# Kernel tuning notes

Measured on AMD Instinct MI355X. Metric: run time of the kernel, lower is better.

## Reference

```python
import jax, jax.numpy as jnp
import numpy as np

EPS = 1e-5  # torch BatchNorm default eps


def _bn(x, gamma, beta, axes):
    # training-mode batch norm over `axes`, channel dim is axis 1
    mean = jnp.mean(x, axis=axes, keepdims=True)
    var = jnp.var(x, axis=axes, keepdims=True)
    shape = [1] * x.ndim
    shape[1] = -1
    return (x - mean) * jax.lax.rsqrt(var + EPS) * gamma.reshape(shape) + beta.reshape(shape)


def setup_inputs() -> dict:
    B, C, N = 16, 512, 192
    S_RATIO, R_RATIO = 4, 8
    Cs, Cr = C // S_RATIO, C // R_RATIO  # 128, 64
    inter = N * Cr + C  # 12800
    key = jax.random.key(0)
    ks = jax.random.split(key, 6)

    def w(k, shp, fan):
        return jax.random.normal(k, shp, jnp.float32) * np.float32(np.sqrt(2.0 / fan))

    return {
        "inputs": jax.random.normal(ks[0], (B, C, N), jnp.float32),
        "retain": 0,
        "theta_w": w(ks[1], (Cs, C), Cs), "theta_b": jnp.zeros((Cs,), jnp.float32),
        "theta_g": jnp.ones((Cs,), jnp.float32), "theta_be": jnp.zeros((Cs,), jnp.float32),
        "phi_w": w(ks[2], (Cs, C), Cs), "phi_b": jnp.zeros((Cs,), jnp.float32),
        "phi_g": jnp.ones((Cs,), jnp.float32), "phi_be": jnp.zeros((Cs,), jnp.float32),
        "re_w": w(ks[3], (Cr, Cs), Cr), "re_b": jnp.zeros((Cr,), jnp.float32),
        "re_g": jnp.ones((Cr,), jnp.float32), "re_be": jnp.zeros((Cr,), jnp.float32),
        "att_w": w(ks[4], (C, inter), C), "att_b": jnp.zeros((C,), jnp.float32),
        "att_g": jnp.ones((C,), jnp.float32), "att_be": jnp.zeros((C,), jnp.float32),
    }


def reference(inputs, retain, theta_w, theta_b, theta_g, theta_be,
              phi_w, phi_b, phi_g, phi_be, re_w, re_b, re_g, re_be,
              att_w, att_b, att_g, att_be):
    B, C, N = inputs.shape
    xt = inputs.transpose(0, 2, 1)  # [B, N, C]

    # theta / phi pro_blocks: Linear -> BN1d (over B,N) -> ReLU, output [B, Cs, N]
    th = jax.nn.relu(_bn(jnp.einsum('bnc,oc->bon', xt, theta_w) + theta_b[None, :, None], theta_g, theta_be, (0, 2)))
    ph = jax.nn.relu(_bn(jnp.einsum('bnc,oc->bon', xt, phi_w) + phi_b[None, :, None], phi_g, phi_be, (0, 2)))
    th = th.transpose(0, 2, 1)  # [B, N, Cs]
    ph = ph.transpose(0, 2, 1)  # [B, N, Cs]

    # pairwise broadcast-diff: [B, N, N, Cs]
    diff = th[:, :, None, :] - ph[:, None, :, :]

    # pro_block1: Linear -> BN2d -> ReLU, then flatten to [B, N, N*Cr]
    rel = jnp.einsum('bijc,oc->boij', diff, re_w) + re_b[None, :, None, None]  # [B, Cr, N, N]
    rel = jax.nn.relu(_bn(rel, re_g, re_be, (0, 2, 3)))
    rel = rel.transpose(0, 2, 3, 1).reshape(B, N, -1)  # [B, N, N*Cr]

    # attention_generator: Linear -> BN1d -> sigmoid, output [B, C, N]
    cat = jnp.concatenate([xt, rel], axis=2)  # [B, N, C + N*Cr]
    att = jnp.einsum('bni,oi->bon', cat, att_w) + att_b[None, :, None]  # [B, C, N]
    att = jax.nn.sigmoid(_bn(att, att_g, att_be, (0, 2)))

    features = att * inputs  # [B, C, N]
    if retain:
        return features
    return jnp.sum(features, axis=2) / jnp.sum(att, axis=2)  # [B, C]
```

## Files before the change

kernel.cpp:

```cpp
#include <hip/hip_runtime.h>

#define BB 16
#define CC 512
#define NN 192
#define CS 128
#define CR 64
#define EPSF 1e-5f
#define PART (BB*CC*NN)

typedef __attribute__((ext_vector_type(8))) short short8;
typedef __attribute__((ext_vector_type(4))) float f32x4;
typedef __attribute__((ext_vector_type(4))) unsigned int uint4v;

#define OFF_LIN2  0
#define OFF_P2    786432
#define OFF_QT    983040
#define OFF_ATTP4 1179648
#define OFF_WBF   7471104
#define OFF_XT    10747904
#define OFF_ROWS  11534336
#define OFF_SPART 11567104

__device__ __forceinline__ unsigned pkbf(float a, float b){
  unsigned r; asm("v_cvt_pk_bf16_f32 %0, %1, %2" : "=v"(r) : "v"(a), "v"(b)); return r;
}

__device__ __forceinline__ void gload_lds16(const void* g, void* l){
  __builtin_amdgcn_global_load_lds(
      (const __attribute__((address_space(1))) unsigned int*)g,
      (__attribute__((address_space(3))) unsigned int*)l, 16, 0, 0);
}

__global__ __launch_bounds__(256) void kconvxt(
    const float* __restrict__ aw, const float* __restrict__ x,
    short* __restrict__ wbf, short* __restrict__ xT)
{
  __shared__ float Ts[64][65];
  if (blockIdx.x < 3200) {
    int t = blockIdx.x*256 + threadIdx.x;
    int o2 = t / 1600;
    int kk = (t - o2*1600) * 8;
    const float* src = &aw[o2*12800 + kk];
    float4 v0 = *reinterpret_cast<const float4*>(src);
    float4 v1 = *reinterpret_cast<const float4*>(src+4);
    uint4v w;
    w.x = pkbf(v0.x, v0.y); w.y = pkbf(v0.z, v0.w);
    w.z = pkbf(v1.x, v1.y); w.w = pkbf(v1.z, v1.w);
    *reinterpret_cast<uint4v*>(&wbf[o2*12800 + kk]) = w;
  } else {
    int bid = blockIdx.x - 3200;
    int nt = bid % 3; int ct = (bid/3) & 7; int b = bid / 24;
    int c0 = ct*64, n0 = nt*64;
    int tid = threadIdx.x;
    int col = tid & 63, r0 = tid >> 6;
    #pragma unroll
    for (int it = 0; it < 16; ++it){
      int r = r0 + it*4;
      Ts[r][col] = x[(b*CC + c0 + r)*NN + n0 + col];
    }
    __syncthreads();
    #pragma unroll
    for (int it = 0; it < 2; ++it){
      int cp = it*256 + tid;
      int nr = cp >> 3, cc8 = (cp & 7)*8;
      uint4v wv;
      wv.x = pkbf(Ts[cc8+0][nr], Ts[cc8+1][nr]);
      wv.y = pkbf(Ts[cc8+2][nr], Ts[cc8+3][nr]);
      wv.z = pkbf(Ts[cc8+4][nr], Ts[cc8+5][nr]);
      wv.w = pkbf(Ts[cc8+6][nr], Ts[cc8+7][nr]);
      *reinterpret_cast<uint4v*>(&xT[((b*NN) + n0 + nr)*CC + c0 + cc8]) = wv;
    }
  }
}

__global__ __launch_bounds__(256) void k1_lin(
    const float* __restrict__ x, const float* __restrict__ wth,
    const float* __restrict__ wph, float* __restrict__ lin2,
    float* __restrict__ spart)
{
  int bid = blockIdx.x;
  int nt = bid % 3; int ch = (bid/3) & 3; int b = (bid/12) & 15; int path = bid/192;
  int cs0 = ch*32, n0 = nt*64;
  const float* w = path ? wph : wth;
  int tid = threadIdx.x;
  int ty = tid >> 4, tx = tid & 15;
  __shared__ float Xs[32][64];
  __shared__ float Ws[32][36];
  float acc[2][4];
  #pragma unroll
  for (int i=0;i<2;++i)
    #pragma unroll
    for (int j=0;j<4;++j) acc[i][j]=0.f;
  for (int c0 = 0; c0 < CC; c0 += 32){
    __syncthreads();
    {
      int nn = tid & 63, cb = tid >> 6;
      #pragma unroll
      for (int it = 0; it < 8; ++it)
        Xs[cb + it*4][nn] = x[(b*CC + c0 + cb + it*4)*NN + n0 + nn];
    }
    {
      int cc = tid & 31, sb = tid >> 5;
      #pragma unroll
      for (int it = 0; it < 4; ++it)
        Ws[cc][sb + it*8] = w[(cs0 + sb + it*8)*CC + c0 + cc];
    }
    __syncthreads();
    #pragma unroll 8
    for (int cc = 0; cc < 32; ++cc){
      float w2[2], x4[4];
      w2[0] = Ws[cc][ty*2]; w2[1] = Ws[cc][ty*2+1];
      *reinterpret_cast<float4*>(x4) = *reinterpret_cast<const float4*>(&Xs[cc][tx*4]);
      #pragma unroll
      for (int i=0;i<2;++i)
        #pragma unroll
        for (int j=0;j<4;++j) acc[i][j] += w2[i]*x4[j];
    }
  }
  #pragma unroll
  for (int r = 0; r < 2; ++r){
    int cs = cs0 + ty*2 + r;
    float4 v = make_float4(acc[r][0],acc[r][1],acc[r][2],acc[r][3]);
    *reinterpret_cast<float4*>(&lin2[(b*256 + path*128 + cs)*NN + n0 + tx*4]) = v;
  }
  #pragma unroll
  for (int r = 0; r < 2; ++r){
    float s = acc[r][0]+acc[r][1]+acc[r][2]+acc[r][3];
    float q = acc[r][0]*acc[r][0]+acc[r][1]*acc[r][1]
            + acc[r][2]*acc[r][2]+acc[r][3]*acc[r][3];
    #pragma unroll
    for (int off=8; off; off>>=1){ s += __shfl_down(s,off,16); q += __shfl_down(q,off,16); }
    if (tx==0){
      int cs2 = path*128 + cs0 + ty*2 + r;
      spart[cs2*48 + b*3 + nt] = s;
      spart[12288 + cs2*48 + b*3 + nt] = q;
    }
  }
}

__global__ __launch_bounds__(256) void k3_gemm(
    const float* __restrict__ lin2, const float* __restrict__ spart,
    const float* __restrict__ tg, const float* __restrict__ tbe,
    const float* __restrict__ pg, const float* __restrict__ pbe,
    const float* __restrict__ rw,
    float* __restrict__ p2raw, float* __restrict__ qTraw,
    float* __restrict__ rows8)
{
  int bid = blockIdx.x;
  int ih = bid & 7; int b = (bid>>3) & 15; int path = bid >> 7;
  int i0 = ih*24;
  __shared__ float Ls[128][24];
  __shared__ float Ws[64][132];
  __shared__ float sscl[512];
  int tid = threadIdx.x;
  {
    int c2 = tid;
    float s=0.f, q=0.f;
    #pragma unroll 8
    for (int i=0;i<48;++i){ s += spart[c2*48+i]; q += spart[12288+c2*48+i]; }
    float mean = s * (1.f/3072.f);
    float var = q * (1.f/3072.f) - mean*mean;
    int pth = c2 >> 7, c = c2 & 127;
    float g  = pth ? pg[c]  : tg[c];
    float be = pth ? pbe[c] : tbe[c];
    float a = g * rsqrtf(var + EPSF);
    sscl[c2] = a; sscl[256+c2] = be - mean*a;
  }
  __syncthreads();
  #pragma unroll
  for (int it = 0; it < 3; ++it){
    int cp = it*256 + tid;
    int row = cp / 6, c4 = cp - row*6;
    float a = sscl[path*128 + row], d = sscl[256 + path*128 + row];
    float4 v = *reinterpret_cast<const float4*>(&lin2[(b*256 + path*128 + row)*NN + i0 + c4*4]);
    float4 r;
    r.x = fmaxf(a*v.x + d, 0.f); r.y = fmaxf(a*v.y + d, 0.f);
    r.z = fmaxf(a*v.z + d, 0.f); r.w = fmaxf(a*v.w + d, 0.f);
    *reinterpret_cast<float4*>(&Ls[row][c4*4]) = r;
  }
  #pragma unroll
  for (int it = 0; it < 8; ++it){
    int cp = it*256 + tid;
    int o = cp >> 5, c4 = cp & 31;
    *reinterpret_cast<float4*>(&Ws[o][c4*4]) =
      *reinterpret_cast<const float4*>(&rw[o*CS + c4*4]);
  }
  __syncthreads();
  int oy = tid >> 3, ix = tid & 7;
  float acc[2][3];
  #pragma unroll
  for (int r=0;r<2;++r)
    #pragma unroll
    for (int e=0;e<3;++e) acc[r][e]=0.f;
  #pragma unroll 4
  for (int c = 0; c < 128; ++c){
    float w2[2], l3[3];
    #pragma unroll
    for (int r=0;r<2;++r) w2[r] = Ws[oy*2+r][c];
    #pragma unroll
    for (int e=0;e<3;++e) l3[e] = Ls[c][ix*3+e];
    #pragma unroll
    for (int r=0;r<2;++r)
      #pragma unroll
      for (int e=0;e<3;++e) acc[r][e] += w2[r]*l3[e];
  }
  float* dst = path ? qTraw : p2raw;
  #pragma unroll
  for (int r=0;r<2;++r)
    #pragma unroll
    for (int e=0;e<3;++e)
      dst[(b*NN + i0 + ix*3 + e)*64 + oy*2 + r] = acc[r][e];
  #pragma unroll
  for (int r=0;r<2;++r){
    float s = acc[r][0]+acc[r][1]+acc[r][2];
    float q = acc[r][0]*acc[r][0]+acc[r][1]*acc[r][1]+acc[r][2]*acc[r][2];
    #pragma unroll
    for (int off=4; off; off>>=1){ s += __shfl_down(s,off,8); q += __shfl_down(q,off,8); }
    if (ix==0){
      int o = oy*2+r;
      int ri = (path*1024 + b*64 + o)*8 + ih;
      rows8[ri] = s; rows8[16384 + ri] = q;
    }
  }
}

__global__ __launch_bounds__(256) void k5_mfma(
    const short* __restrict__ wbf, const short* __restrict__ xT,
    const float* __restrict__ p2raw, const float* __restrict__ qTraw,
    const float* __restrict__ rows8,
    const float* __restrict__ rg, const float* __restrict__ rbe,
    float* __restrict__ attp4)
{
  int bid = blockIdx.x;
  int nt = bid & 1, mt = (bid >> 1) & 3, b = (bid >> 3) & 15, ks = bid >> 7;
  int o20 = mt*128, n0 = nt*96;
  int j0 = ks*48;

  int tid = threadIdx.x;
  int w = tid >> 6, lane = tid & 63;
  int wr = w >> 1, wc = w & 1;
  int l15 = lane & 15, l4 = lane >> 4;
  int cq = tid & 7;

  __shared__ __align__(16) short As[2][128*64];
  __shared__ __align__(16) short Bs[96*64];
  __shared__ __align__(16) float qall[48*64];
  __shared__ float srel[128];
  __shared__ float sred[4][5][64];

  {
    int o = tid & 63, g = tid >> 6;
    float sa=0,sb=0,saq=0,sbq=0,cross=0;
    #pragma unroll
    for (int bb=g*4; bb<g*4+4; ++bb){
      float ra=0, rb=0;
      #pragma unroll
      for (int ih=0; ih<8; ++ih){
        int ia = (bb*64+o)*8 + ih, ib = (1024 + bb*64+o)*8 + ih;
        ra += rows8[ia]; rb += rows8[ib];
        saq += rows8[16384 + ia]; sbq += rows8[16384 + ib];
      }
      sa += ra; sb += rb; cross += ra*rb;
    }
    sred[g][0][o]=sa; sred[g][1][o]=sb; sred[g][2][o]=saq;
    sred[g][3][o]=sbq; sred[g][4][o]=cross;
  }
  {
    const float* qsrc = &qTraw[(size_t)(b*NN + j0)*64];
    #pragma unroll
    for (int it=0; it<3; ++it){
      int cp = it*256 + tid;
      gload_lds16(qsrc + cp*4, &qall[cp*4]);
    }
  }
  __syncthreads();
  if (tid < 64){
    int o = tid;
    float sa=0,sb=0,saq=0,sbq=0,cross=0;
    #pragma unroll
    for (int g=0; g<4; ++g){
      sa += sred[g][0][o]; sb += sred[g][1][o]; saq += sred[g][2][o];
      sbq += sred[g][3][o]; cross += sred[g][4][o];
    }
    float mean = (sa - sb) * (1.f/3072.f);
    float e2 = (saq + sbq) * (1.f/3072.f) - cross * (2.f/589824.f);
    float var = e2 - mean*mean;
    float s = rg[o] * rsqrtf(var + EPSF);
    srel[o] = s;
    srel[64+o] = rbe[o] - s*mean;
  }
  __syncthreads();

  float pr[3][8];
  {
    float sc8[8], sh8[8];
    #pragma unroll
    for (int k=0;k<8;++k){ sc8[k] = srel[cq*8+k]; sh8[k] = srel[64+cq*8+k]; }
    #pragma unroll
    for (int it=0; it<3; ++it){
      int n = it*32 + (tid >> 3);
      const float* pp = &p2raw[(size_t)((b*NN) + n0 + n)*64 + cq*8];
      float4 u0 = *reinterpret_cast<const float4*>(pp);
      float4 u1 = *reinterpret_cast<const float4*>(pp+4);
      pr[it][0]=sc8[0]*u0.x+sh8[0]; pr[it][1]=sc8[1]*u0.y+sh8[1];
      pr[it][2]=sc8[2]*u0.z+sh8[2]; pr[it][3]=sc8[3]*u0.w+sh8[3];
      pr[it][4]=sc8[4]*u1.x+sh8[4]; pr[it][5]=sc8[5]*u1.y+sh8[5];
      pr[it][6]=sc8[6]*u1.z+sh8[6]; pr[it][7]=sc8[7]*u1.w+sh8[7];
    }
  }

  auto stageA = [&](int buf, int colbase){
    #pragma unroll
    for (int it=0; it<4; ++it){
      int cp = w*256 + it*64 + lane;
      int row = cp >> 3, c = (cp & 7) ^ (row & 7);
      gload_lds16(&wbf[(o20 + row)*12800 + colbase + c*8],
                  &As[buf][(w*256 + it*64)*8]);
    }
  };
  auto stageBx = [&](int colbase){
    #pragma unroll
    for (int it=0; it<3; ++it){
      int cp = w*192 + it*64 + lane;
      int row = cp >> 3, c = (cp & 7) ^ (row & 7);
      gload_lds16(&xT[(size_t)((b*NN) + n0 + row)*CC + colbase + c*8],
                  &Bs[(w*192 + it*64)*8]);
    }
  };

  f32x4 acc[4][3];
  #pragma unroll
  for (int mi=0;mi<4;++mi)
    #pragma unroll
    for (int ni=0;ni<3;++ni) acc[mi][ni] = (f32x4){0.f,0.f,0.f,0.f};

  auto mfma_phase = [&](int buf){
    __builtin_amdgcn_s_setprio(1);
    #pragma unroll
    for (int s=0; s<2; ++s){
      short8 av[4], bv[3];
      int c = s*4 + l4;
      #pragma unroll
      for (int mi=0; mi<4; ++mi){
        int row = wr*64 + mi*16 + l15;
        av[mi] = *reinterpret_cast<const short8*>(&As[buf][row*64 + ((c ^ (row&7))<<3)]);
      }
      #pragma unroll
      for (int ni=0; ni<3; ++ni){
        int rown = wc*48 + ni*16 + l15;
        bv[ni] = *reinterpret_cast<const short8*>(&Bs[rown*64 + ((c ^ (rown&7))<<3)]);
      }
      #pragma unroll
      for (int mi=0; mi<4; ++mi)
        #pragma unroll
        for (int ni=0; ni<3; ++ni)
          acc[mi][ni] = __builtin_amdgcn_mfma_f32_16x16x32_bf16(av[mi], bv[ni], acc[mi][ni], 0, 0, 0);
    }
    __builtin_amdgcn_s_setprio(0);
  };

  #pragma unroll
  for (int kt = 0; kt < 2; ++kt){
    __syncthreads();
    stageA(0, ks*128 + kt*64);
    stageBx(ks*128 + kt*64);
    if (kt == 0){
      #pragma unroll
      for (int it=0; it<12; ++it){
        int i = it*256 + tid;
        qall[i] *= srel[i & 63];
      }
    }
    __syncthreads();
    mfma_phase(0);
  }

  __syncthreads();
  stageA(0, 512 + j0*64);
  for (int kt = 0; kt < 48; ++kt){
    int cur = kt & 1;
    if (kt < 47) stageA(cur^1, 512 + (j0 + kt + 1)*64);
    {
      const float* qq = &qall[kt*64];
      float4 qa = *reinterpret_cast<const float4*>(&qq[cq*8]);
      float4 qb = *reinterpret_cast<const float4*>(&qq[cq*8+4]);
      #pragma unroll
      for (int it=0; it<3; ++it){
        float r0 = fmaxf(pr[it][0]-qa.x, 0.f);
        float r1 = fmaxf(pr[it][1]-qa.y, 0.f);
        float r2 = fmaxf(pr[it][2]-qa.z, 0.f);
        float r3 = fmaxf(pr[it][3]-qa.w, 0.f);
        float r4 = fmaxf(pr[it][4]-qb.x, 0.f);
        float r5 = fmaxf(pr[it][5]-qb.y, 0.f);
        float r6 = fmaxf(pr[it][6]-qb.z, 0.f);
        float r7 = fmaxf(pr[it][7]-qb.w, 0.f);
        uint4v wv;
        wv.x = pkbf(r0,r1); wv.y = pkbf(r2,r3);
        wv.z = pkbf(r4,r5); wv.w = pkbf(r6,r7);
        int n = it*32 + (tid >> 3);
        *reinterpret_cast<uint4v*>(&Bs[n*64 + ((cq ^ (n&7))<<3)]) = wv;
      }
    }
    if (kt < 47) asm volatile("s_waitcnt vmcnt(4) lgkmcnt(0)" ::: "memory");
    else         asm volatile("s_waitcnt vmcnt(0) lgkmcnt(0)" ::: "memory");
    __builtin_amdgcn_sched_barrier(0);
    __builtin_amdgcn_s_barrier();
    mfma_phase(cur);
    __builtin_amdgcn_s_barrier();
  }

  float* dst = attp4 + (size_t)ks*PART;
  #pragma unroll
  for (int mi=0; mi<4; ++mi){
    #pragma unroll
    for (int r=0; r<4; ++r){
      int o2 = o20 + wr*64 + mi*16 + l4*4 + r;
      #pragma unroll
      for (int ni=0; ni<3; ++ni){
        int n = n0 + wc*48 + ni*16 + l15;
        dst[(b*CC + o2)*NN + n] = acc[mi][ni][r];
      }
    }
  }
}

__global__ __launch_bounds__(256) void k67(
    const float* __restrict__ p4, const float* __restrict__ x,
    const float* __restrict__ g, const float* __restrict__ be,
    float* __restrict__ out)
{
  int o2 = blockIdx.x;
  int tid = threadIdx.x;
  int b = tid >> 4, nl = tid & 15;
  float v[12], xv[12];
  float s=0.f, q=0.f;
  #pragma unroll
  for (int it=0; it<6; ++it){
    int n = nl*2 + it*32;
    int idx = (b*CC + o2)*NN + n;
    float t0=0.f, t1=0.f;
    #pragma unroll
    for (int p=0; p<4; ++p){
      float2 u = *reinterpret_cast<const float2*>(&p4[(size_t)p*PART + idx]);
      t0 += u.x; t1 += u.y;
    }
    float2 xu = *reinterpret_cast<const float2*>(&x[idx]);
    v[it*2] = t0; v[it*2+1] = t1;
    xv[it*2] = xu.x; xv[it*2+1] = xu.y;
    s += t0 + t1; q += t0*t0 + t1*t1;
  }
  __shared__ float rs[4], rq[4], ad[2];
  #pragma unroll
  for (int off=32; off; off>>=1){ s += __shfl_down(s,off); q += __shfl_down(q,off); }
  int w = tid >> 6;
  if ((tid & 63)==0){ rs[w]=s; rq[w]=q; }
  __syncthreads();
  if (tid==0){
    s = rs[0]+rs[1]+rs[2]+rs[3]; q = rq[0]+rq[1]+rq[2]+rq[3];
    float mean = s * (1.f/3072.f);
    float var = q * (1.f/3072.f) - mean*mean;
    float a = g[o2] * rsqrtf(var + EPSF);
    ad[0] = a; ad[1] = be[o2] - mean*a;
  }
  __syncthreads();
  float a = ad[0], d = ad[1];
  float sf=0.f, ss=0.f;
  #pragma unroll
  for (int it=0; it<12; ++it){
    float sig = 1.f/(1.f + expf(-(a*v[it] + d)));
    sf += sig * xv[it]; ss += sig;
  }
  #pragma unroll
  for (int off=8; off; off>>=1){ sf += __shfl_down(sf,off,16); ss += __shfl_down(ss,off,16); }
  if (nl==0) out[b*CC + o2] = sf/ss;
}

extern "C" void kernel_launch(void* const* d_in, const int* in_sizes, int n_in,
                              void* d_out, int out_size, void* d_ws, size_t ws_size,
                              hipStream_t stream)
{
  const float* inputs  = (const float*)d_in[0];
  const float* theta_w = (const float*)d_in[2];
  const float* theta_g = (const float*)d_in[4];
  const float* theta_be= (const float*)d_in[5];
  const float* phi_w   = (const float*)d_in[6];
  const float* phi_g   = (const float*)d_in[8];
  const float* phi_be  = (const float*)d_in[9];
  const float* re_w    = (const float*)d_in[10];
  const float* re_g    = (const float*)d_in[12];
  const float* re_be   = (const float*)d_in[13];
  const float* att_w   = (const float*)d_in[14];
  const float* att_g   = (const float*)d_in[16];
  const float* att_be  = (const float*)d_in[17];

  float* ws = (float*)d_ws;
  float* lin2  = ws + OFF_LIN2;
  float* p2raw = ws + OFF_P2;
  float* qTraw = ws + OFF_QT;
  float* attp4 = ws + OFF_ATTP4;
  short* wbf   = (short*)(ws + OFF_WBF);
  short* xT    = (short*)(ws + OFF_XT);
  float* rows8 = ws + OFF_ROWS;
  float* spart = ws + OFF_SPART;

  kconvxt<<<3584, 256, 0, stream>>>(att_w, inputs, wbf, xT);
  k1_lin<<<384, 256, 0, stream>>>(inputs, theta_w, phi_w, lin2, spart);
  k3_gemm<<<256, 256, 0, stream>>>(lin2, spart, theta_g, theta_be, phi_g, phi_be,
                                   re_w, p2raw, qTraw, rows8);
  k5_mfma<<<512, 256, 0, stream>>>(wbf, xT, p2raw, qTraw, rows8, re_g, re_be, attp4);
  k67<<<512, 256, 0, stream>>>(attp4, inputs, att_g, att_be, (float*)d_out);
}
```

Measured before the change: 118.7 us.

## Merge theta/phi paths in k1 and widen k5 tiles to full N

k1_lin now computes both the theta and phi projections in one block, so each X tile is loaded once and shared by both, which halves the grid. k5_mfma switches to 512-thread blocks that cover all 192 columns, so each A (weight) tile is staged once per block instead of once per column half, and the relation tile B is built once. The cost is fewer blocks on both launches (192 and 256), which lowers occupancy and parallelism on a large GPU, plus larger LDS use per k5 block.

After: 131.5 us. +10.7%, slower.

```diff
diff --git a/kernel.cpp b/kernel.cpp
--- a/kernel.cpp
+++ b/kernel.cpp
@@ -79,18 +79,20 @@
     float* __restrict__ spart)
 {
   int bid = blockIdx.x;
-  int nt = bid % 3; int ch = (bid/3) & 3; int b = (bid/12) & 15; int path = bid/192;
+  int nt = bid % 3; int ch = (bid/3) & 3; int b = bid/12;
   int cs0 = ch*32, n0 = nt*64;
-  const float* w = path ? wph : wth;
   int tid = threadIdx.x;
   int ty = tid >> 4, tx = tid & 15;
   __shared__ float Xs[32][64];
-  __shared__ float Ws[32][36];
-  float acc[2][4];
-  #pragma unroll
-  for (int i=0;i<2;++i)
-    #pragma unroll
-    for (int j=0;j<4;++j) acc[i][j]=0.f;
+  __shared__ float Wt[32][36];
+  __shared__ float Wp[32][36];
+  float acc[2][2][4];
+  #pragma unroll
+  for (int p=0;p<2;++p)
+    #pragma unroll
+    for (int i=0;i<2;++i)
+      #pragma unroll
+      for (int j=0;j<4;++j) acc[p][i][j]=0.f;
   for (int c0 = 0; c0 < CC; c0 += 32){
     __syncthreads();
     {
@@ -102,38 +104,44 @@
     {
       int cc = tid & 31, sb = tid >> 5;
       #pragma unroll
-      for (int it = 0; it < 4; ++it)
-        Ws[cc][sb + it*8] = w[(cs0 + sb + it*8)*CC + c0 + cc];
+      for (int it = 0; it < 4; ++it){
+        Wt[cc][sb + it*8] = wth[(cs0 + sb + it*8)*CC + c0 + cc];
+        Wp[cc][sb + it*8] = wph[(cs0 + sb + it*8)*CC + c0 + cc];
+      }
     }
     __syncthreads();
     #pragma unroll 8
     for (int cc = 0; cc < 32; ++cc){
-      float w2[2], x4[4];
-      w2[0] = Ws[cc][ty*2]; w2[1] = Ws[cc][ty*2+1];
+      float wt2[2], wp2[2], x4[4];
+      wt2[0] = Wt[cc][ty*2]; wt2[1] = Wt[cc][ty*2+1];
+      wp2[0] = Wp[cc][ty*2]; wp2[1] = Wp[cc][ty*2+1];
       *reinterpret_cast<float4*>(x4) = *reinterpret_cast<const float4*>(&Xs[cc][tx*4]);
       #pragma unroll
       for (int i=0;i<2;++i)
         #pragma unroll
-        for (int j=0;j<4;++j) acc[i][j] += w2[i]*x4[j];
-    }
-  }
-  #pragma unroll
-  for (int r = 0; r < 2; ++r){
-    int cs = cs0 + ty*2 + r;
-    float4 v = make_float4(acc[r][0],acc[r][1],acc[r][2],acc[r][3]);
-    *reinterpret_cast<float4*>(&lin2[(b*256 + path*128 + cs)*NN + n0 + tx*4]) = v;
-  }
-  #pragma unroll
-  for (int r = 0; r < 2; ++r){
-    float s = acc[r][0]+acc[r][1]+acc[r][2]+acc[r][3];
-    float q = acc[r][0]*acc[r][0]+acc[r][1]*acc[r][1]
-            + acc[r][2]*acc[r][2]+acc[r][3]*acc[r][3];
-    #pragma unroll
-    for (int off=8; off; off>>=1){ s += __shfl_down(s,off,16); q += __shfl_down(q,off,16); }
-    if (tx==0){
-      int cs2 = path*128 + cs0 + ty*2 + r;
-      spart[cs2*48 + b*3 + nt] = s;
-      spart[12288 + cs2*48 + b*3 + nt] = q;
+        for (int j=0;j<4;++j){
+          acc[0][i][j] += wt2[i]*x4[j];
+          acc[1][i][j] += wp2[i]*x4[j];
+        }
+    }
+  }
+  #pragma unroll
+  for (int p = 0; p < 2; ++p){
+    #pragma unroll
+    for (int r = 0; r < 2; ++r){
+      int cs = cs0 + ty*2 + r;
+      float4 v = make_float4(acc[p][r][0],acc[p][r][1],acc[p][r][2],acc[p][r][3]);
+      *reinterpret_cast<float4*>(&lin2[(b*256 + p*128 + cs)*NN + n0 + tx*4]) = v;
+      float s = acc[p][r][0]+acc[p][r][1]+acc[p][r][2]+acc[p][r][3];
+      float q = acc[p][r][0]*acc[p][r][0]+acc[p][r][1]*acc[p][r][1]
+              + acc[p][r][2]*acc[p][r][2]+acc[p][r][3]*acc[p][r][3];
+      #pragma unroll
+      for (int off=8; off; off>>=1){ s += __shfl_down(s,off,16); q += __shfl_down(q,off,16); }
+      if (tx==0){
+        int cs2 = p*128 + cs;
+        spart[cs2*48 + b*3 + nt] = s;
+        spart[12288 + cs2*48 + b*3 + nt] = q;
+      }
     }
   }
 }
@@ -224,7 +232,7 @@
   }
 }
 
-__global__ __launch_bounds__(256) void k5_mfma(
+__global__ __launch_bounds__(512) void k5_mfma(
     const short* __restrict__ wbf, const short* __restrict__ xT,
     const float* __restrict__ p2raw, const float* __restrict__ qTraw,
     const float* __restrict__ rows8,
@@ -232,27 +240,27 @@
     float* __restrict__ attp4)
 {
   int bid = blockIdx.x;
-  int nt = bid & 1, mt = (bid >> 1) & 3, b = (bid >> 3) & 15, ks = bid >> 7;
-  int o20 = mt*128, n0 = nt*96;
+  int mt = bid & 3, b = (bid >> 2) & 15, ks = bid >> 6;
+  int o20 = mt*128;
   int j0 = ks*48;
 
   int tid = threadIdx.x;
   int w = tid >> 6, lane = tid & 63;
-  int wr = w >> 1, wc = w & 1;
+  int wr = w >> 2, wc = w & 3;
   int l15 = lane & 15, l4 = lane >> 4;
   int cq = tid & 7;
 
   __shared__ __align__(16) short As[2][128*64];
-  __shared__ __align__(16) short Bs[96*64];
+  __shared__ __align__(16) short Bs[192*64];
   __shared__ __align__(16) float qall[48*64];
   __shared__ float srel[128];
-  __shared__ float sred[4][5][64];
+  __shared__ float sred[8][5][64];
 
   {
     int o = tid & 63, g = tid >> 6;
     float sa=0,sb=0,saq=0,sbq=0,cross=0;
     #pragma unroll
-    for (int bb=g*4; bb<g*4+4; ++bb){
+    for (int bb=g*2; bb<g*2+2; ++bb){
       float ra=0, rb=0;
       #pragma unroll
       for (int ih=0; ih<8; ++ih){
@@ -267,18 +275,15 @@
   }
   {
     const float* qsrc = &qTraw[(size_t)(b*NN + j0)*64];
-    #pragma unroll
-    for (int it=0; it<3; ++it){
-      int cp = it*256 + tid;
-      gload_lds16(qsrc + cp*4, &qall[cp*4]);
-    }
+    gload_lds16(qsrc + tid*4, &qall[tid*4]);
+    if (tid < 256) gload_lds16(qsrc + (512+tid)*4, &qall[(512+tid)*4]);
   }
   __syncthreads();
   if (tid < 64){
     int o = tid;
     float sa=0,sb=0,saq=0,sbq=0,cross=0;
     #pragma unroll
-    for (int g=0; g<4; ++g){
+    for (int g=0; g<8; ++g){
       sa += sred[g][0][o]; sb += sred[g][1][o]; saq += sred[g][2][o];
       sbq += sred[g][3][o]; cross += sred[g][4][o];
     }
@@ -298,8 +303,8 @@
     for (int k=0;k<8;++k){ sc8[k] = srel[cq*8+k]; sh8[k] = srel[64+cq*8+k]; }
     #pragma unroll
     for (int it=0; it<3; ++it){
-      int n = it*32 + (tid >> 3);
-      const float* pp = &p2raw[(size_t)((b*NN) + n0 + n)*64 + cq*8];
+      int n = it*64 + (tid >> 3);
+      const float* pp = &p2raw[(size_t)((b*NN) + n)*64 + cq*8];
       float4 u0 = *reinterpret_cast<const float4*>(pp);
       float4 u1 = *reinterpret_cast<const float4*>(pp+4);
       pr[it][0]=sc8[0]*u0.x+sh8[0]; pr[it][1]=sc8[1]*u0.y+sh8[1];
@@ -311,11 +316,11 @@
 
   auto stageA = [&](int buf, int colbase){
     #pragma unroll
-    for (int it=0; it<4; ++it){
-      int cp = w*256 + it*64 + lane;
+    for (int it=0; it<2; ++it){
+      int cp = w*128 + it*64 + lane;
       int row = cp >> 3, c = (cp & 7) ^ (row & 7);
       gload_lds16(&wbf[(o20 + row)*12800 + colbase + c*8],
-                  &As[buf][(w*256 + it*64)*8]);
+                  &As[buf][(w*128 + it*64)*8]);
     }
   };
   auto stageBx = [&](int colbase){
@@ -323,7 +328,7 @@
     for (int it=0; it<3; ++it){
       int cp = w*192 + it*64 + lane;
       int row = cp >> 3, c = (cp & 7) ^ (row & 7);
-      gload_lds16(&xT[(size_t)((b*NN) + n0 + row)*CC + colbase + c*8],
+      gload_lds16(&xT[(size_t)((b*NN) + row)*CC + colbase + c*8],
                   &Bs[(w*192 + it*64)*8]);
     }
   };
@@ -366,8 +371,8 @@
     stageBx(ks*128 + kt*64);
     if (kt == 0){
       #pragma unroll
-      for (int it=0; it<12; ++it){
-        int i = it*256 + tid;
+      for (int it=0; it<6; ++it){
+        int i = it*512 + tid;
         qall[i] *= srel[i & 63];
       }
     }
@@ -397,11 +402,11 @@
         uint4v wv;
         wv.x = pkbf(r0,r1); wv.y = pkbf(r2,r3);
         wv.z = pkbf(r4,r5); wv.w = pkbf(r6,r7);
-        int n = it*32 + (tid >> 3);
+        int n = it*64 + (tid >> 3);
         *reinterpret_cast<uint4v*>(&Bs[n*64 + ((cq ^ (n&7))<<3)]) = wv;
       }
     }
-    if (kt < 47) asm volatile("s_waitcnt vmcnt(4) lgkmcnt(0)" ::: "memory");
+    if (kt < 47) asm volatile("s_waitcnt vmcnt(2) lgkmcnt(0)" ::: "memory");
     else         asm volatile("s_waitcnt vmcnt(0) lgkmcnt(0)" ::: "memory");
     __builtin_amdgcn_sched_barrier(0);
     __builtin_amdgcn_s_barrier();
@@ -417,7 +422,7 @@
       int o2 = o20 + wr*64 + mi*16 + l4*4 + r;
       #pragma unroll
       for (int ni=0; ni<3; ++ni){
-        int n = n0 + wc*48 + ni*16 + l15;
+        int n = wc*48 + ni*16 + l15;
         dst[(b*CC + o2)*NN + n] = acc[mi][ni][r];
       }
     }
@@ -504,9 +509,9 @@
   float* spart = ws + OFF_SPART;
 
   kconvxt<<<3584, 256, 0, stream>>>(att_w, inputs, wbf, xT);
-  k1_lin<<<384, 256, 0, stream>>>(inputs, theta_w, phi_w, lin2, spart);
+  k1_lin<<<192, 256, 0, stream>>>(inputs, theta_w, phi_w, lin2, spart);
   k3_gemm<<<256, 256, 0, stream>>>(lin2, spart, theta_g, theta_be, phi_g, phi_be,
                                    re_w, p2raw, qTraw, rows8);
-  k5_mfma<<<512, 256, 0, stream>>>(wbf, xT, p2raw, qTraw, rows8, re_g, re_be, attp4);
+  k5_mfma<<<256, 512, 0, stream>>>(wbf, xT, p2raw, qTraw, rows8, re_g, re_be, attp4);
   k67<<<512, 256, 0, stream>>>(attp4, inputs, att_g, att_be, (float*)d_out);
 }
```
